# Kernel tuning notes

Measured on AMD Instinct MI355X. Metric: run time of the kernel, lower is better.

The kernel has to match this reference:

```python
import jax, jax.numpy as jnp
import numpy as np

N_NODES = 50000
IN_CH = 256
OUT_CH = 128
HID = 2 * OUT_CH  # 256
N_EDGES = 800000


def setup_inputs() -> dict:
    key = jax.random.key(0)
    ks = jax.random.split(key, 12)
    glorot = lambda k, shape: jax.random.normal(k, shape, jnp.float32) * (2.0 / sum(shape)) ** 0.5
    return {
        "x": jax.random.normal(ks[0], (N_NODES, IN_CH), jnp.float32),
        "edge_index": jax.random.randint(ks[1], (2, N_EDGES), 0, N_NODES),
        "conv_w": glorot(ks[2], (IN_CH, HID)),      # MetaGCNConv weight: x @ W
        "conv_b": jnp.zeros((HID,), jnp.float32),
        "fc1_w": glorot(ks[3], (HID, HID)), "fc1_b": jnp.zeros((HID,), jnp.float32),
        "fc2_w": glorot(ks[4], (HID, HID)), "fc2_b": jnp.zeros((HID,), jnp.float32),
        "fc3_w": glorot(ks[5], (OUT_CH, HID)), "fc3_b": jnp.zeros((OUT_CH,), jnp.float32),
        "fc4_w": glorot(ks[6], (OUT_CH, HID)), "fc4_b": jnp.zeros((OUT_CH,), jnp.float32),
    }


def reference(x, edge_index, conv_w, conv_b, fc1_w, fc1_b, fc2_w, fc2_b, fc3_w, fc3_b, fc4_w, fc4_b):
    N = x.shape[0]
    # GCN with added self-loops and symmetric normalization (PyG GCNConv semantics)
    loop = jnp.arange(N)
    src = jnp.concatenate([edge_index[0], loop])
    dst = jnp.concatenate([edge_index[1], loop])
    xw = x @ conv_w  # [N, HID]
    ones = jnp.ones_like(src, dtype=x.dtype)
    deg = jax.ops.segment_sum(ones, src, num_segments=N)
    dinv = jnp.where(deg > 0, jax.lax.rsqrt(deg), 0.0)
    norm = dinv[src] * dinv[dst]  # [E+N]
    agg = jax.ops.segment_sum(norm[:, None] * xw[src], dst, num_segments=N)  # [N, HID]
    h = jax.nn.relu(agg + conv_b)
    s = h.sum(0)  # [HID]
    lin = lambda v, w, b: jnp.tanh(v @ w.T + b)
    return (lin(s, fc1_w, fc1_b), lin(s, fc2_w, fc2_b), lin(s, fc3_w, fc3_b), lin(s, fc4_w, fc4_b))
```

## Files before the change

kernel.cpp:

```cpp
#include <hip/hip_runtime.h>
#include <math.h>

#define CH 256
#define BCAP 64

typedef short bf16x8 __attribute__((ext_vector_type(8)));
typedef float f32x4 __attribute__((ext_vector_type(4)));
typedef unsigned int u32;

__device__ __forceinline__ unsigned short f2bf(float f) {
    u32 u = __float_as_uint(f);
    u += 0x7FFFu + ((u >> 16) & 1u);
    return (unsigned short)(u >> 16);
}
__device__ __forceinline__ float bf2f(unsigned short h) {
    return __uint_as_float(((u32)h) << 16);
}
__device__ __forceinline__ float lo16f(u32 q) { return __uint_as_float(q << 16); }
__device__ __forceinline__ float hi16f(u32 q) { return __uint_as_float(q & 0xffff0000u); }
__device__ __forceinline__ void async16(const void* g, void* l) {
    __builtin_amdgcn_global_load_lds((const __attribute__((address_space(1))) u32*)g,
                                     (__attribute__((address_space(3))) u32*)l, 16, 0, 0);
}

__global__ __launch_bounds__(256) void prep_kernel(const float* __restrict__ x,
                                                   unsigned short* __restrict__ xb,
                                                   const float* __restrict__ W,
                                                   unsigned short* __restrict__ whiT,
                                                   unsigned short* __restrict__ wloT,
                                                   int N) {
    int b = blockIdx.x, t = threadIdx.x;
    if (b < 1024) {
        long long total8 = (long long)N * CH / 8;
        long long i = (long long)b * 256 + t;
        long long stride = 1024LL * 256;
        const float4* src = (const float4*)x;
        for (; i < total8; i += stride) {
            float4 a = src[i * 2], c = src[i * 2 + 1];
            ushort4 o0, o1;
            o0.x = f2bf(a.x); o0.y = f2bf(a.y); o0.z = f2bf(a.z); o0.w = f2bf(a.w);
            o1.x = f2bf(c.x); o1.y = f2bf(c.y); o1.z = f2bf(c.z); o1.w = f2bf(c.w);
            ((ushort4*)xb)[i * 2]     = o0;
            ((ushort4*)xb)[i * 2 + 1] = o1;
        }
    } else {
        int b2 = b - 1024;
#pragma unroll
        for (int i = 0; i < 4; i++) {
            int n = b2 * 4 + i;
            float w = W[(size_t)t * CH + n];
            unsigned short hi = f2bf(w);
            unsigned short lo = f2bf(w - bf2f(hi));
            whiT[(size_t)n * CH + t] = hi;
            wloT[(size_t)n * CH + t] = lo;
        }
    }
}

__global__ void fill_kernel(const int* __restrict__ ei,
                            unsigned* __restrict__ cnt_src,
                            unsigned* __restrict__ cnt_dst,
                            unsigned* __restrict__ col, int E) {
    int i = blockIdx.x * blockDim.x + threadIdx.x;
    int stride = gridDim.x * blockDim.x;
    for (; i < E; i += stride) {
        int s = ei[i];
        int d = ei[E + i];
        atomicAdd(&cnt_src[s], 1u);
        unsigned pos = atomicAdd(&cnt_dst[d], 1u);
        if (pos < BCAP) col[(size_t)d * BCAP + pos] = (unsigned)s;
    }
}

__global__ __launch_bounds__(256) void gemm_mfma(const unsigned short* __restrict__ xb,
                                                 const unsigned short* __restrict__ whiT,
                                                 const unsigned short* __restrict__ wloT,
                                                 const unsigned* __restrict__ cnt_src,
                                                 unsigned short* __restrict__ y, int M) {
    __shared__ __align__(16) unsigned short smA [128 * 32];
    __shared__ __align__(16) unsigned short smBh[128 * 32];
    __shared__ __align__(16) unsigned short smBl[128 * 32];
    int t = threadIdx.x;
    int lane = t & 63, w = t >> 6;
    int m0 = blockIdx.x * 128;
    int n0 = blockIdx.y * 128;
    int mo = (w >> 1) * 64, no = (w & 1) * 64;
    int quad = lane >> 4, l16 = lane & 15;

    f32x4 acc[4][4] = {};

    int idx0 = t, idx1 = t + 256;
    int rA0 = idx0 >> 2, kq0 = idx0 & 3;
    int rA1 = idx1 >> 2, kq1 = idx1 & 3;
    int gm0 = min(m0 + rA0, M - 1), gm1 = min(m0 + rA1, M - 1);
    size_t ga0 = (size_t)gm0 * CH + kq0 * 8;
    size_t ga1 = (size_t)gm1 * CH + kq1 * 8;
    size_t gb0 = (size_t)(n0 + rA0) * CH + kq0 * 8;
    size_t gb1 = (size_t)(n0 + rA1) * CH + kq1 * 8;

    for (int k0 = 0; k0 < CH; k0 += 32) {
        async16(&xb  [ga0 + k0], &smA [idx0 * 8]);
        async16(&xb  [ga1 + k0], &smA [idx1 * 8]);
        async16(&whiT[gb0 + k0], &smBh[idx0 * 8]);
        async16(&whiT[gb1 + k0], &smBh[idx1 * 8]);
        async16(&wloT[gb0 + k0], &smBl[idx0 * 8]);
        async16(&wloT[gb1 + k0], &smBl[idx1 * 8]);
        __syncthreads();

        bf16x8 a[4], bh[4], bl[4];
#pragma unroll
        for (int i = 0; i < 4; i++)
            a[i] = *(const bf16x8*)&smA[(mo + i * 16 + l16) * 32 + quad * 8];
#pragma unroll
        for (int j = 0; j < 4; j++) {
            bh[j] = *(const bf16x8*)&smBh[(no + j * 16 + l16) * 32 + quad * 8];
            bl[j] = *(const bf16x8*)&smBl[(no + j * 16 + l16) * 32 + quad * 8];
        }
#pragma unroll
        for (int i = 0; i < 4; i++)
#pragma unroll
            for (int j = 0; j < 4; j++) {
                acc[i][j] = __builtin_amdgcn_mfma_f32_16x16x32_bf16(a[i], bh[j], acc[i][j], 0, 0, 0);
                acc[i][j] = __builtin_amdgcn_mfma_f32_16x16x32_bf16(a[i], bl[j], acc[i][j], 0, 0, 0);
            }
        __syncthreads();
    }

#pragma unroll
    for (int i = 0; i < 4; i++) {
        int mbase = m0 + mo + i * 16 + quad * 4;
#pragma unroll
        for (int r = 0; r < 4; r++) {
            int m = mbase + r;
            if (m < M) {
                float dv = rsqrtf((float)(cnt_src[m] + 1u));
#pragma unroll
                for (int j = 0; j < 4; j++) {
                    int ncol = n0 + no + j * 16 + l16;
                    int s = ncol >> 5, c = ncol & 31;
                    y[((size_t)s * M + m) * 32 + c] = f2bf(dv * acc[i][j][r]);
                }
            }
        }
    }
}

__global__ __launch_bounds__(256) void gather_kernel(const unsigned short* __restrict__ y,
                                                     const unsigned* __restrict__ cnt_src,
                                                     const unsigned* __restrict__ cnt_dst,
                                                     const unsigned* __restrict__ col,
                                                     const float* __restrict__ bias,
                                                     float* __restrict__ s_sum, int N) {
    int t = threadIdx.x;
    int lane = t & 63, wv = t >> 6;
    int slice = blockIdx.x & 7;
    int grp   = blockIdx.x >> 3;
    int ng = lane >> 4;
    int g  = (lane >> 2) & 3;
    int li = lane & 3;
    const unsigned short* ys = y + (size_t)slice * N * 32;

    float b8[8];
#pragma unroll
    for (int j = 0; j < 8; j++) b8[j] = bias[slice * 32 + li * 8 + j];

    float ts[8] = {0.f, 0.f, 0.f, 0.f, 0.f, 0.f, 0.f, 0.f};

    int wid = grp * 4 + wv;
    int nw  = (gridDim.x >> 3) * 4;

    for (int base = wid * 4; base < N; base += nw * 4) {
        int n = min(base + ng, N - 1);
        unsigned deg = min(cnt_dst[n], (unsigned)BCAP);
        unsigned cnt = deg + 1;
        float gnm = (g == 0 && base + ng < N) ? 1.f : 0.f;
        unsigned mc = cnt;
        mc = max(mc, (unsigned)__shfl_xor((int)mc, 16, 64));
        mc = max(mc, (unsigned)__shfl_xor((int)mc, 32, 64));

        const unsigned* cb = col + (size_t)n * BCAP;
        float acc[8] = {0.f, 0.f, 0.f, 0.f, 0.f, 0.f, 0.f, 0.f};
        for (unsigned k = 0; k < mc; k += 4) {
            unsigned r = k + g;
            unsigned src = (r < deg) ? cb[r] : (unsigned)n;
            float m = (r < cnt) ? 1.f : 0.f;
            uint4 q = *(const uint4*)(ys + (size_t)src * 32 + li * 8);
            acc[0] = fmaf(m, lo16f(q.x), acc[0]);
            acc[1] = fmaf(m, hi16f(q.x), acc[1]);
            acc[2] = fmaf(m, lo16f(q.y), acc[2]);
            acc[3] = fmaf(m, hi16f(q.y), acc[3]);
            acc[4] = fmaf(m, lo16f(q.z), acc[4]);
            acc[5] = fmaf(m, hi16f(q.z), acc[5]);
            acc[6] = fmaf(m, lo16f(q.w), acc[6]);
            acc[7] = fmaf(m, hi16f(q.w), acc[7]);
        }
        float dv = rsqrtf((float)(cnt_src[n] + 1u));
#pragma unroll
        for (int j = 0; j < 8; j++) {
            float v = acc[j];
            v += __shfl_xor(v, 4, 64);
            v += __shfl_xor(v, 8, 64);
            float h = fmaxf(fmaf(dv, v, b8[j]), 0.f);
            ts[j] = fmaf(gnm, h, ts[j]);
        }
    }

#pragma unroll
    for (int j = 0; j < 8; j++) {
        float v = ts[j];
        v += __shfl_xor(v, 16, 64);
        v += __shfl_xor(v, 32, 64);
        ts[j] = v;
    }

    __shared__ float red[4][32];
    if (lane < 4) {
#pragma unroll
        for (int j = 0; j < 8; j++) red[wv][lane * 8 + j] = ts[j];
    }
    __syncthreads();
    if (t < 32) {
        atomicAdd(&s_sum[slice * 32 + t],
                  red[0][t] + red[1][t] + red[2][t] + red[3][t]);
    }
}

__global__ __launch_bounds__(256) void fc_kernel(const float* __restrict__ s_sum,
                                                 const float* __restrict__ fc1_w, const float* __restrict__ fc1_b,
                                                 const float* __restrict__ fc2_w, const float* __restrict__ fc2_b,
                                                 const float* __restrict__ fc3_w, const float* __restrict__ fc3_b,
                                                 const float* __restrict__ fc4_w, const float* __restrict__ fc4_b,
                                                 float* __restrict__ out) {
    int wid  = (blockIdx.x * blockDim.x + threadIdx.x) >> 6;
    int lane = threadIdx.x & 63;
    if (wid >= 768) return;
    const float* w; const float* b; int row, obase;
    if (wid < 256)      { w = fc1_w; b = fc1_b; row = wid;       obase = 0;   }
    else if (wid < 512) { w = fc2_w; b = fc2_b; row = wid - 256; obase = 256; }
    else if (wid < 640) { w = fc3_w; b = fc3_b; row = wid - 512; obase = 512; }
    else                { w = fc4_w; b = fc4_b; row = wid - 640; obase = 640; }
    float4 wv = *(const float4*)&w[(size_t)row * 256 + lane * 4];
    float4 sv = *(const float4*)&s_sum[lane * 4];
    float d = wv.x * sv.x + wv.y * sv.y + wv.z * sv.z + wv.w * sv.w;
#pragma unroll
    for (int off = 32; off; off >>= 1) d += __shfl_down(d, off, 64);
    if (lane == 0) out[obase + row] = tanhf(d + b[row]);
}

extern "C" void kernel_launch(void* const* d_in, const int* in_sizes, int n_in,
                              void* d_out, int out_size, void* d_ws, size_t ws_size,
                              hipStream_t stream) {
    const float* x      = (const float*)d_in[0];
    const int*   ei     = (const int*)d_in[1];
    const float* conv_w = (const float*)d_in[2];
    const float* conv_b = (const float*)d_in[3];
    const float* fc1_w  = (const float*)d_in[4];
    const float* fc1_b  = (const float*)d_in[5];
    const float* fc2_w  = (const float*)d_in[6];
    const float* fc2_b  = (const float*)d_in[7];
    const float* fc3_w  = (const float*)d_in[8];
    const float* fc3_b  = (const float*)d_in[9];
    const float* fc4_w  = (const float*)d_in[10];
    const float* fc4_b  = (const float*)d_in[11];
    float* out = (float*)d_out;

    const int N = in_sizes[0] / CH;
    const int E = in_sizes[1] / 2;

    char* ws = (char*)d_ws;
    size_t off = 0;
    auto alloc = [&](size_t bytes) -> void* {
        off = (off + 255) & ~(size_t)255;
        void* p = ws + off;
        off += bytes;
        return p;
    };
    unsigned* cnt_src = (unsigned*)alloc((size_t)N * 4);
    unsigned* cnt_dst = (unsigned*)alloc((size_t)N * 4);
    float*    s_sum   = (float*)alloc((size_t)CH * 4);
    size_t zero_bytes = off;
    unsigned* col     = (unsigned*)alloc((size_t)N * BCAP * 4);
    unsigned short* xb   = (unsigned short*)alloc((size_t)N * CH * 2);
    unsigned short* whiT = (unsigned short*)alloc((size_t)CH * CH * 2);
    unsigned short* wloT = (unsigned short*)alloc((size_t)CH * CH * 2);
    unsigned short* y    = (unsigned short*)alloc((size_t)N * CH * 2);

    hipMemsetAsync(ws, 0, zero_bytes, stream);

    prep_kernel<<<1088, 256, 0, stream>>>(x, xb, conv_w, whiT, wloT, N);
    fill_kernel<<<1024, 256, 0, stream>>>(ei, cnt_src, cnt_dst, col, E);
    dim3 ggrid((N + 127) / 128, 2);
    gemm_mfma<<<ggrid, 256, 0, stream>>>(xb, whiT, wloT, cnt_src, y, N);
    gather_kernel<<<2048, 256, 0, stream>>>(y, cnt_src, cnt_dst, col, conv_b, s_sum, N);
    fc_kernel<<<192, 256, 0, stream>>>(s_sum,
                                       fc1_w, fc1_b, fc2_w, fc2_b,
                                       fc3_w, fc3_b, fc4_w, fc4_b, out);
}
```

Measured before the change: 278.2 us.

## Fuse bf16 conversion into GEMM and co-schedule edge fill with GEMM blocks

Drops the separate pass that converts x to bf16: the GEMM now loads fp32 x rows, packs them to bf16 in registers and stores them into LDS. The edge-count/CSR fill is folded into the same launch, with GEMM and fill blocks interleaved so atomics overlap MFMA work. The memset moves into the weight-prep kernel. Degree scaling moves out of the GEMM epilogue into a new scale pass over y, which adds an extra read and write of y. The new pkbf packing rounds half-up rather than to nearest-even.

```diff
diff --git a/kernel.cpp b/kernel.cpp
--- a/kernel.cpp
+++ b/kernel.cpp
@@ -18,129 +18,151 @@
 }
 __device__ __forceinline__ float lo16f(u32 q) { return __uint_as_float(q << 16); }
 __device__ __forceinline__ float hi16f(u32 q) { return __uint_as_float(q & 0xffff0000u); }
+__device__ __forceinline__ u32 pkbf(float a, float b) {
+    u32 ua = __float_as_uint(a) + 0x8000u;
+    u32 ub = __float_as_uint(b) + 0x8000u;
+    return __builtin_amdgcn_perm(ub, ua, 0x07060302u);
+}
 __device__ __forceinline__ void async16(const void* g, void* l) {
     __builtin_amdgcn_global_load_lds((const __attribute__((address_space(1))) u32*)g,
                                      (__attribute__((address_space(3))) u32*)l, 16, 0, 0);
 }
 
-__global__ __launch_bounds__(256) void prep_kernel(const float* __restrict__ x,
-                                                   unsigned short* __restrict__ xb,
-                                                   const float* __restrict__ W,
+__global__ __launch_bounds__(256) void prep_kernel(const float* __restrict__ W,
                                                    unsigned short* __restrict__ whiT,
                                                    unsigned short* __restrict__ wloT,
-                                                   int N) {
+                                                   float4* __restrict__ zbase,
+                                                   int zcount4) {
     int b = blockIdx.x, t = threadIdx.x;
-    if (b < 1024) {
-        long long total8 = (long long)N * CH / 8;
-        long long i = (long long)b * 256 + t;
-        long long stride = 1024LL * 256;
-        const float4* src = (const float4*)x;
-        for (; i < total8; i += stride) {
-            float4 a = src[i * 2], c = src[i * 2 + 1];
-            ushort4 o0, o1;
-            o0.x = f2bf(a.x); o0.y = f2bf(a.y); o0.z = f2bf(a.z); o0.w = f2bf(a.w);
-            o1.x = f2bf(c.x); o1.y = f2bf(c.y); o1.z = f2bf(c.z); o1.w = f2bf(c.w);
-            ((ushort4*)xb)[i * 2]     = o0;
-            ((ushort4*)xb)[i * 2 + 1] = o1;
-        }
-    } else {
-        int b2 = b - 1024;
+    if (b < 64) {
 #pragma unroll
         for (int i = 0; i < 4; i++) {
-            int n = b2 * 4 + i;
+            int n = b * 4 + i;
             float w = W[(size_t)t * CH + n];
             unsigned short hi = f2bf(w);
             unsigned short lo = f2bf(w - bf2f(hi));
             whiT[(size_t)n * CH + t] = hi;
             wloT[(size_t)n * CH + t] = lo;
         }
-    }
-}
-
-__global__ void fill_kernel(const int* __restrict__ ei,
-                            unsigned* __restrict__ cnt_src,
-                            unsigned* __restrict__ cnt_dst,
-                            unsigned* __restrict__ col, int E) {
-    int i = blockIdx.x * blockDim.x + threadIdx.x;
-    int stride = gridDim.x * blockDim.x;
-    for (; i < E; i += stride) {
-        int s = ei[i];
-        int d = ei[E + i];
-        atomicAdd(&cnt_src[s], 1u);
-        unsigned pos = atomicAdd(&cnt_dst[d], 1u);
-        if (pos < BCAP) col[(size_t)d * BCAP + pos] = (unsigned)s;
-    }
-}
-
-__global__ __launch_bounds__(256) void gemm_mfma(const unsigned short* __restrict__ xb,
-                                                 const unsigned short* __restrict__ whiT,
-                                                 const unsigned short* __restrict__ wloT,
-                                                 const unsigned* __restrict__ cnt_src,
-                                                 unsigned short* __restrict__ y, int M) {
-    __shared__ __align__(16) unsigned short smA [128 * 32];
-    __shared__ __align__(16) unsigned short smBh[128 * 32];
-    __shared__ __align__(16) unsigned short smBl[128 * 32];
-    int t = threadIdx.x;
-    int lane = t & 63, w = t >> 6;
-    int m0 = blockIdx.x * 128;
-    int n0 = blockIdx.y * 128;
-    int mo = (w >> 1) * 64, no = (w & 1) * 64;
-    int quad = lane >> 4, l16 = lane & 15;
-
-    f32x4 acc[4][4] = {};
-
-    int idx0 = t, idx1 = t + 256;
-    int rA0 = idx0 >> 2, kq0 = idx0 & 3;
-    int rA1 = idx1 >> 2, kq1 = idx1 & 3;
-    int gm0 = min(m0 + rA0, M - 1), gm1 = min(m0 + rA1, M - 1);
-    size_t ga0 = (size_t)gm0 * CH + kq0 * 8;
-    size_t ga1 = (size_t)gm1 * CH + kq1 * 8;
-    size_t gb0 = (size_t)(n0 + rA0) * CH + kq0 * 8;
-    size_t gb1 = (size_t)(n0 + rA1) * CH + kq1 * 8;
-
-    for (int k0 = 0; k0 < CH; k0 += 32) {
-        async16(&xb  [ga0 + k0], &smA [idx0 * 8]);
-        async16(&xb  [ga1 + k0], &smA [idx1 * 8]);
-        async16(&whiT[gb0 + k0], &smBh[idx0 * 8]);
-        async16(&whiT[gb1 + k0], &smBh[idx1 * 8]);
-        async16(&wloT[gb0 + k0], &smBl[idx0 * 8]);
-        async16(&wloT[gb1 + k0], &smBl[idx1 * 8]);
-        __syncthreads();
-
-        bf16x8 a[4], bh[4], bl[4];
-#pragma unroll
-        for (int i = 0; i < 4; i++)
-            a[i] = *(const bf16x8*)&smA[(mo + i * 16 + l16) * 32 + quad * 8];
-#pragma unroll
-        for (int j = 0; j < 4; j++) {
-            bh[j] = *(const bf16x8*)&smBh[(no + j * 16 + l16) * 32 + quad * 8];
-            bl[j] = *(const bf16x8*)&smBl[(no + j * 16 + l16) * 32 + quad * 8];
-        }
-#pragma unroll
-        for (int i = 0; i < 4; i++)
+    } else {
+        int i = (b - 64) * 256 + t;
+        int stride = 104 * 256;
+        float4 z = make_float4(0.f, 0.f, 0.f, 0.f);
+        for (; i < zcount4; i += stride) zbase[i] = z;
+    }
+}
+
+__global__ __launch_bounds__(256) void mega_kernel(const float* __restrict__ x,
+                                                   const unsigned short* __restrict__ whiT,
+                                                   const unsigned short* __restrict__ wloT,
+                                                   const int* __restrict__ ei,
+                                                   unsigned* __restrict__ cnt_src,
+                                                   unsigned* __restrict__ cnt_dst,
+                                                   unsigned* __restrict__ col,
+                                                   unsigned short* __restrict__ y,
+                                                   int M, int E, int G) {
+    int b = blockIdx.x, t = threadIdx.x;
+    if (b < 2 * G && !(b & 1)) {
+        __shared__ __align__(16) unsigned short smA [128 * 32];
+        __shared__ __align__(16) unsigned short smBh[128 * 32];
+        __shared__ __align__(16) unsigned short smBl[128 * 32];
+        int g = b >> 1;
+        int lane = t & 63, w = t >> 6;
+        int m0 = (g >> 1) * 128;
+        int n0 = (g & 1) * 128;
+        int mo = (w >> 1) * 64, no = (w & 1) * 64;
+        int quad = lane >> 4, l16 = lane & 15;
+
+        f32x4 acc[4][4] = {};
+
+        int arow = t >> 1, ahalf = t & 1;
+        int gm = min(m0 + arow, M - 1);
+        const float* xrow = x + (size_t)gm * CH + ahalf * 16;
+        int idx0 = t, idx1 = t + 256;
+        size_t gb0 = (size_t)(n0 + (idx0 >> 2)) * CH + (idx0 & 3) * 8;
+        size_t gb1 = (size_t)(n0 + (idx1 >> 2)) * CH + (idx1 & 3) * 8;
+
+        for (int k0 = 0; k0 < CH; k0 += 32) {
+            const float4* xp = (const float4*)(xrow + k0);
+            float4 v0 = xp[0], v1 = xp[1], v2 = xp[2], v3 = xp[3];
+            async16(&whiT[gb0 + k0], &smBh[idx0 * 8]);
+            async16(&whiT[gb1 + k0], &smBh[idx1 * 8]);
+            async16(&wloT[gb0 + k0], &smBl[idx0 * 8]);
+            async16(&wloT[gb1 + k0], &smBl[idx1 * 8]);
+            uint4 w0 = make_uint4(pkbf(v0.x, v0.y), pkbf(v0.z, v0.w),
+                                  pkbf(v1.x, v1.y), pkbf(v1.z, v1.w));
+            uint4 w1 = make_uint4(pkbf(v2.x, v2.y), pkbf(v2.z, v2.w),
+                                  pkbf(v3.x, v3.y), pkbf(v3.z, v3.w));
+            *(uint4*)&smA[arow * 32 + ahalf * 16]     = w0;
+            *(uint4*)&smA[arow * 32 + ahalf * 16 + 8] = w1;
+            __syncthreads();
+
+            bf16x8 a[4], bh[4], bl[4];
+#pragma unroll
+            for (int i = 0; i < 4; i++)
+                a[i] = *(const bf16x8*)&smA[(mo + i * 16 + l16) * 32 + quad * 8];
 #pragma unroll
             for (int j = 0; j < 4; j++) {
-                acc[i][j] = __builtin_amdgcn_mfma_f32_16x16x32_bf16(a[i], bh[j], acc[i][j], 0, 0, 0);
-                acc[i][j] = __builtin_amdgcn_mfma_f32_16x16x32_bf16(a[i], bl[j], acc[i][j], 0, 0, 0);
+                bh[j] = *(const bf16x8*)&smBh[(no + j * 16 + l16) * 32 + quad * 8];
+                bl[j] = *(const bf16x8*)&smBl[(no + j * 16 + l16) * 32 + quad * 8];
             }
-        __syncthreads();
-    }
-
-#pragma unroll
-    for (int i = 0; i < 4; i++) {
-        int mbase = m0 + mo + i * 16 + quad * 4;
-#pragma unroll
-        for (int r = 0; r < 4; r++) {
-            int m = mbase + r;
-            if (m < M) {
-                float dv = rsqrtf((float)(cnt_src[m] + 1u));
+#pragma unroll
+            for (int i = 0; i < 4; i++)
 #pragma unroll
                 for (int j = 0; j < 4; j++) {
-                    int ncol = n0 + no + j * 16 + l16;
-                    int s = ncol >> 5, c = ncol & 31;
-                    y[((size_t)s * M + m) * 32 + c] = f2bf(dv * acc[i][j][r]);
+                    acc[i][j] = __builtin_amdgcn_mfma_f32_16x16x32_bf16(a[i], bh[j], acc[i][j], 0, 0, 0);
+                    acc[i][j] = __builtin_amdgcn_mfma_f32_16x16x32_bf16(a[i], bl[j], acc[i][j], 0, 0, 0);
+                }
+            __syncthreads();
+        }
+#pragma unroll
+        for (int i = 0; i < 4; i++) {
+            int mbase = m0 + mo + i * 16 + quad * 4;
+#pragma unroll
+            for (int r = 0; r < 4; r++) {
+                int m = mbase + r;
+                if (m < M) {
+#pragma unroll
+                    for (int j = 0; j < 4; j++) {
+                        int ncol = n0 + no + j * 16 + l16;
+                        int s = ncol >> 5, c = ncol & 31;
+                        y[((size_t)s * M + m) * 32 + c] = f2bf(acc[i][j][r]);
+                    }
                 }
             }
+        }
+    } else {
+        int fb = (b < 2 * G) ? (b >> 1) : (b - G);
+        if (fb >= 1024) return;
+        int i = fb * 256 + t;
+        int stride = 1024 * 256;
+        for (; i < E; i += stride) {
+            int s = ei[i];
+            int d = ei[E + i];
+            atomicAdd(&cnt_src[s], 1u);
+            unsigned pos = atomicAdd(&cnt_dst[d], 1u);
+            if (pos < BCAP) col[(size_t)d * BCAP + pos] = (unsigned)s;
+        }
+    }
+}
+
+__global__ __launch_bounds__(256) void scale_kernel(unsigned short* __restrict__ y,
+                                                    const unsigned* __restrict__ cnt_src,
+                                                    int M) {
+    int gid = blockIdx.x * 256 + threadIdx.x;
+    int gstride = gridDim.x * 256;
+    int total4 = M * 4;
+    uint4* yq = (uint4*)y;
+    for (int s = 0; s < 8; s++) {
+        for (int c = gid; c < total4; c += gstride) {
+            int m = c >> 2;
+            float dv = rsqrtf((float)(cnt_src[m] + 1u));
+            uint4 q = yq[(size_t)s * total4 + c];
+            q.x = pkbf(dv * lo16f(q.x), dv * hi16f(q.x));
+            q.y = pkbf(dv * lo16f(q.y), dv * hi16f(q.y));
+            q.z = pkbf(dv * lo16f(q.z), dv * hi16f(q.z));
+            q.w = pkbf(dv * lo16f(q.w), dv * hi16f(q.w));
+            yq[(size_t)s * total4 + c] = q;
         }
     }
 }
@@ -266,6 +288,7 @@
 
     const int N = in_sizes[0] / CH;
     const int E = in_sizes[1] / 2;
+    const int G = ((N + 127) / 128) * 2;
 
     char* ws = (char*)d_ws;
     size_t off = 0;
@@ -280,17 +303,16 @@
     float*    s_sum   = (float*)alloc((size_t)CH * 4);
     size_t zero_bytes = off;
     unsigned* col     = (unsigned*)alloc((size_t)N * BCAP * 4);
-    unsigned short* xb   = (unsigned short*)alloc((size_t)N * CH * 2);
     unsigned short* whiT = (unsigned short*)alloc((size_t)CH * CH * 2);
     unsigned short* wloT = (unsigned short*)alloc((size_t)CH * CH * 2);
     unsigned short* y    = (unsigned short*)alloc((size_t)N * CH * 2);
 
-    hipMemsetAsync(ws, 0, zero_bytes, stream);
-
-    prep_kernel<<<1088, 256, 0, stream>>>(x, xb, conv_w, whiT, wloT, N);
-    fill_kernel<<<1024, 256, 0, stream>>>(ei, cnt_src, cnt_dst, col, E);
-    dim3 ggrid((N + 127) / 128, 2);
-    gemm_mfma<<<ggrid, 256, 0, stream>>>(xb, whiT, wloT, cnt_src, y, N);
+    int zcount4 = (int)((zero_bytes + 15) / 16);
+
+    prep_kernel<<<168, 256, 0, stream>>>(conv_w, whiT, wloT, (float4*)ws, zcount4);
+    mega_kernel<<<G + 1024, 256, 0, stream>>>(x, whiT, wloT, ei,
+                                              cnt_src, cnt_dst, col, y, N, E, G);
+    scale_kernel<<<1024, 256, 0, stream>>>(y, cnt_src, N);
     gather_kernel<<<2048, 256, 0, stream>>>(y, cnt_src, cnt_dst, col, conv_b, s_sum, N);
     fc_kernel<<<192, 256, 0, stream>>>(s_sum,
                                        fc1_w, fc1_b, fc2_w, fc2_b,
```

Measured after the change: 243.9 us. 1.14x faster.
